# Kernel optimization log

Measured on AMD Instinct MI355X. Metric: run time of the kernel, lower is better.

The kernel has to match this reference:

```python
import jax, jax.numpy as jnp
import numpy as np

C = 1024      # channels
K = 7         # kernel_size
G = 1         # groups (G>1 crashes in the original torch code; see notes)
GC = C // G   # group_channels
OFFSET_SCALE = 2.0
LN_EPS = 1e-5


def setup_inputs() -> dict:
    key = jax.random.key(0)
    ks = jax.random.split(key, 8)
    N, L = 4, 2048
    s = 1.0 / np.sqrt(C)
    x = jax.random.normal(ks[0], (N, L, C), jnp.float32)
    Wi = jax.random.normal(ks[1], (C, C), jnp.float32) * s
    bi = jnp.zeros((C,), jnp.float32)
    dw_w = jax.random.normal(ks[2], (C, 1, 3), jnp.float32) * 0.5   # depthwise conv kernel (O, I/g=1, W)
    dw_b = jnp.zeros((C,), jnp.float32)
    ln_g = jnp.ones((C,), jnp.float32)
    ln_b = jnp.zeros((C,), jnp.float32)
    Wo = jax.random.normal(ks[3], (G * K, C), jnp.float32) * 0.02   # offset head (nonzero to exercise gather)
    bo = jnp.zeros((G * K,), jnp.float32)
    Wm = jax.random.normal(ks[4], (G * K, C), jnp.float32) * 0.02   # mask head
    bm = jnp.zeros((G * K,), jnp.float32)
    Wout = jax.random.normal(ks[5], (C, C), jnp.float32) * s
    bout = jnp.zeros((C,), jnp.float32)
    return {"x": x, "Wi": Wi, "bi": bi, "dw_w": dw_w, "dw_b": dw_b,
            "ln_g": ln_g, "ln_b": ln_b, "Wo": Wo, "bo": bo,
            "Wm": Wm, "bm": bm, "Wout": Wout, "bout": bout}


def _forward(x, Wi, bi, dw_w, dw_b, ln_g, ln_b, Wo, bo, Wm, bm, Wout, bout):
    N, L, Cc = x.shape
    dt = x.dtype
    # input projection
    x_proj = x @ Wi.T + bi                                  # [N,L,C]
    # depthwise conv (k=3, pad=1, groups=C) -> LayerNorm(C) -> GELU(exact)
    y = jax.lax.conv_general_dilated(
        x.transpose(0, 2, 1), dw_w, window_strides=(1,), padding=((1, 1),),
        dimension_numbers=("NCH", "OIH", "NCH"), feature_group_count=Cc)
    x_dw = y.transpose(0, 2, 1) + dw_b                       # [N,L,C]
    mu = x_dw.mean(-1, keepdims=True)
    var = ((x_dw - mu) ** 2).mean(-1, keepdims=True)
    x_dw = (x_dw - mu) * jax.lax.rsqrt(var + LN_EPS) * ln_g + ln_b
    x_dw = jax.nn.gelu(x_dw, approximate=False)
    # dynamic offsets and sampling mask
    offsets = (x_dw @ Wo.T + bo).reshape(N, L, G, K) * OFFSET_SCALE
    mask = jax.nn.softmax((x_dw @ Wm.T + bm).reshape(N, L, G, K), axis=-1)
    mask = jnp.nan_to_num(mask, nan=0.0)
    # absolute sampling positions
    ref_off = jnp.linspace(-(K // 2), K // 2, K).astype(dt)          # [K]
    pos = jnp.arange(L, dtype=dt)[None, :, None, None]               # [1,L,1,1]
    abs_pos = pos + ref_off[None, None, None, :] + offsets           # [N,L,G,K]
    apc = jnp.clip(abs_pos, 0.0, L - 1)
    p_floor = jnp.clip(apc.astype(jnp.int32), 0, L - 1)
    p_ceil = jnp.clip(p_floor + 1, 0, L - 1)
    w_ceil = apc - p_floor.astype(dt)
    w_floor = 1.0 - w_ceil
    valid = jnp.logical_not((abs_pos < 0) | (abs_pos > L - 1)).astype(dt)
    w_floor = w_floor * valid
    w_ceil = w_ceil * valid
    # gather + bilinear blend (G=1: each sample index grabs the full C channels)
    idx_f = p_floor.reshape(N, -1)[:, :, None]                       # [N, L*G*K, 1]
    idx_c = p_ceil.reshape(N, -1)[:, :, None]
    v_floor = jnp.take_along_axis(x_proj, idx_f, axis=1).reshape(N, L, G, K, GC)
    v_ceil = jnp.take_along_axis(x_proj, idx_c, axis=1).reshape(N, L, G, K, GC)
    sampled = v_floor * w_floor[..., None] + v_ceil * w_ceil[..., None]
    out = (sampled * mask[..., None]).sum(axis=3).reshape(N, L, Cc)  # sum over K
    return out @ Wout.T + bout


def reference(x, Wi, bi, dw_w, dw_b, ln_g, ln_b, Wo, bo, Wm, bm, Wout, bout):
    return _forward(x, Wi, bi, dw_w, dw_b, ln_g, ln_b, Wo, bo, Wm, bm, Wout, bout)
```

## Files before the change

### kernel.cpp

```cpp
#include <hip/hip_runtime.h>
#include <hip/hip_bf16.h>
#include <cstdint>

#define C_DIM 1024
#define L_DIM 2048
#define N_DIM 4
#define M_DIM (N_DIM * L_DIM)

typedef __attribute__((ext_vector_type(8))) short frag8;
typedef __attribute__((ext_vector_type(4)))  float f32x4;
typedef __attribute__((ext_vector_type(16))) float f32x16;

__device__ __forceinline__ void gl_lds16(const void* g, void* l) {
  __builtin_amdgcn_global_load_lds((const __attribute__((address_space(1))) void*)g,
                                   (__attribute__((address_space(3))) void*)l,
                                   16, 0, 0);
}
__device__ __forceinline__ void store_out(float* Y, size_t idx, float v) { Y[idx] = v; }
__device__ __forceinline__ void store_out(__hip_bfloat16* Y, size_t idx, float v) {
  Y[idx] = __float2bfloat16(v);
}
__device__ __forceinline__ float4 ldbf4(const __hip_bfloat16* p) {
  union { short4 s; __hip_bfloat16 h[4]; } u; u.s = *(const short4*)p;
  return make_float4((float)u.h[0], (float)u.h[1], (float)u.h[2], (float)u.h[3]);
}
__device__ __forceinline__ void stbf4(__hip_bfloat16* p, float4 v) {
  union { short4 s; __hip_bfloat16 h[4]; } u;
  u.h[0] = __float2bfloat16(v.x); u.h[1] = __float2bfloat16(v.y);
  u.h[2] = __float2bfloat16(v.z); u.h[3] = __float2bfloat16(v.w);
  *(short4*)p = u.s;
}
__device__ __forceinline__ float gelu_fast(float t) {
  const float t3 = t * t * t;
  const float ns = -1.5957691216f * t - 0.0713548163f * t3;
  return t / (1.f + __expf(ns));
}

__global__ __launch_bounds__(256)
void cvt_f32_bf16(const float* __restrict__ in, __hip_bfloat16* __restrict__ out, int n8) {
  const int i = blockIdx.x * 256 + threadIdx.x;
  if (i >= n8) return;
  const float4 a = *(const float4*)(in + (size_t)i * 8);
  const float4 b = *(const float4*)(in + (size_t)i * 8 + 4);
  union { __hip_bfloat16 h[8]; int4 q; } u;
  u.h[0] = __float2bfloat16(a.x); u.h[1] = __float2bfloat16(a.y);
  u.h[2] = __float2bfloat16(a.z); u.h[3] = __float2bfloat16(a.w);
  u.h[4] = __float2bfloat16(b.x); u.h[5] = __float2bfloat16(b.y);
  u.h[6] = __float2bfloat16(b.z); u.h[7] = __float2bfloat16(b.w);
  *(int4*)(out + (size_t)i * 8) = u.q;
}

__global__ __launch_bounds__(256)
void cvt_two_f32_bf16(const float* __restrict__ inA, __hip_bfloat16* __restrict__ outA,
                      const float* __restrict__ inB, __hip_bfloat16* __restrict__ outB,
                      int n8each) {
  int i = blockIdx.x * 256 + threadIdx.x;
  const float* in; __hip_bfloat16* out;
  if (i < n8each) { in = inA; out = outA; }
  else            { in = inB; out = outB; i -= n8each; }
  if (i >= n8each) return;
  const float4 a = *(const float4*)(in + (size_t)i * 8);
  const float4 b = *(const float4*)(in + (size_t)i * 8 + 4);
  union { __hip_bfloat16 h[8]; int4 q; } u;
  u.h[0] = __float2bfloat16(a.x); u.h[1] = __float2bfloat16(a.y);
  u.h[2] = __float2bfloat16(a.z); u.h[3] = __float2bfloat16(a.w);
  u.h[4] = __float2bfloat16(b.x); u.h[5] = __float2bfloat16(b.y);
  u.h[6] = __float2bfloat16(b.z); u.h[7] = __float2bfloat16(b.w);
  *(int4*)(out + (size_t)i * 8) = u.q;
}

template <typename TY>
__global__ __launch_bounds__(256, 2)
void gemm_db(const __hip_bfloat16* __restrict__ X,
             const __hip_bfloat16* __restrict__ W,
             const float* __restrict__ bias,
             TY* __restrict__ Y, int M, int N, int K)
{
  __shared__ __hip_bfloat16 As[2][2][128 * 32];
  __shared__ __hip_bfloat16 Bs[2][2][128 * 32];
  const int tid  = threadIdx.x;
  const int lane = tid & 63;
  const int wave = tid >> 6;
  const int bm = blockIdx.x * 128;
  const int bn = blockIdx.y * 128;
  const int wr = (wave >> 1) * 64;
  const int wc = (wave & 1) * 64;
  const int srow  = tid >> 2;
  const int skoff = (tid & 3) * 8;

  const __hip_bfloat16* gA0 = X + (size_t)(bm + srow) * K + skoff;
  const __hip_bfloat16* gA1 = X + (size_t)(bm + 64 + srow) * K + skoff;
  const __hip_bfloat16* gB0 = W + (size_t)(bn + srow) * K + skoff;
  const __hip_bfloat16* gB1 = W + (size_t)(bn + 64 + srow) * K + skoff;

  f32x16 acc[2][2] = {};
  const int arow  = lane & 31;
  const int akoff = (lane >> 5) * 8;

#define STAGE(k0, buf)                                        \
  do {                                                        \
    gl_lds16(gA0 + (k0),      &As[buf][0][tid * 8]);          \
    gl_lds16(gA1 + (k0),      &As[buf][0][2048 + tid * 8]);   \
    gl_lds16(gA0 + (k0) + 32, &As[buf][1][tid * 8]);          \
    gl_lds16(gA1 + (k0) + 32, &As[buf][1][2048 + tid * 8]);   \
    gl_lds16(gB0 + (k0),      &Bs[buf][0][tid * 8]);          \
    gl_lds16(gB1 + (k0),      &Bs[buf][0][2048 + tid * 8]);   \
    gl_lds16(gB0 + (k0) + 32, &Bs[buf][1][tid * 8]);          \
    gl_lds16(gB1 + (k0) + 32, &Bs[buf][1][2048 + tid * 8]);   \
  } while (0)

  STAGE(0, 0);
  __syncthreads();
  const int iters = K / 64;
  for (int it = 0; it < iters; ++it) {
    const int cur = it & 1;
    if (it + 1 < iters) STAGE((it + 1) * 64, cur ^ 1);

#pragma unroll
    for (int p = 0; p < 2; ++p)
#pragma unroll
      for (int h = 0; h < 2; ++h) {
        const frag8 a0 = *(const frag8*)&As[cur][p][(wr + arow) * 32 + h * 16 + akoff];
        const frag8 a1 = *(const frag8*)&As[cur][p][(wr + 32 + arow) * 32 + h * 16 + akoff];
        const frag8 b0 = *(const frag8*)&Bs[cur][p][(wc + arow) * 32 + h * 16 + akoff];
        const frag8 b1 = *(const frag8*)&Bs[cur][p][(wc + 32 + arow) * 32 + h * 16 + akoff];
        acc[0][0] = __builtin_amdgcn_mfma_f32_32x32x16_bf16(a0, b0, acc[0][0], 0, 0, 0);
        acc[0][1] = __builtin_amdgcn_mfma_f32_32x32x16_bf16(a0, b1, acc[0][1], 0, 0, 0);
        acc[1][0] = __builtin_amdgcn_mfma_f32_32x32x16_bf16(a1, b0, acc[1][0], 0, 0, 0);
        acc[1][1] = __builtin_amdgcn_mfma_f32_32x32x16_bf16(a1, b1, acc[1][1], 0, 0, 0);
      }
    __syncthreads();
  }
#undef STAGE

#pragma unroll
  for (int i = 0; i < 2; i++)
#pragma unroll
    for (int j = 0; j < 2; j++) {
      const int col = bn + wc + j * 32 + (lane & 31);
      const float bv = bias[col];
#pragma unroll
      for (int r = 0; r < 16; r++) {
        const int row = bm + wr + i * 32 + (r & 3) + 8 * (r >> 2) + 4 * (lane >> 5);
        store_out(Y, (size_t)row * N + col, acc[i][j][r] + bv);
      }
    }
}

struct Ld8f { float4 a, b; };
struct Ld8b { int4 a; };
__device__ __forceinline__ Ld8f ld8(const float* p) {
  return { *(const float4*)p, *(const float4*)(p + 4) };
}
__device__ __forceinline__ Ld8b ld8(const __hip_bfloat16* p) { return { *(const int4*)p }; }
__device__ __forceinline__ void st8(__hip_bfloat16* l, const Ld8f& v) {
  union { __hip_bfloat16 h[8]; int4 q; } u;
  u.h[0] = __float2bfloat16(v.a.x); u.h[1] = __float2bfloat16(v.a.y);
  u.h[2] = __float2bfloat16(v.a.z); u.h[3] = __float2bfloat16(v.a.w);
  u.h[4] = __float2bfloat16(v.b.x); u.h[5] = __float2bfloat16(v.b.y);
  u.h[6] = __float2bfloat16(v.b.z); u.h[7] = __float2bfloat16(v.b.w);
  *(int4*)l = u.q;
}
__device__ __forceinline__ void st8(__hip_bfloat16* l, const Ld8b& v) { *(int4*)l = v.a; }

template <typename TX, typename TY>
__global__ __launch_bounds__(256, 2)
void gemm_nt(const TX* __restrict__ X, const float* __restrict__ W,
             const float* __restrict__ bias, TY* __restrict__ Y, int M, int N, int K)
{
  __shared__ __hip_bfloat16 As[128 * 32];
  __shared__ __hip_bfloat16 Bs[128 * 32];
  const int tid  = threadIdx.x;
  const int lane = tid & 63;
  const int wave = tid >> 6;
  const int bm = blockIdx.x * 128;
  const int bn = blockIdx.y * 128;
  const int wr = (wave >> 1) * 64;
  const int wc = (wave & 1) * 64;
  const int srow  = tid >> 2;
  const int skoff = (tid & 3) * 8;

  f32x4 acc[4][4] = {};
  const TX*    gA0 = X + (size_t)(bm + srow) * K + skoff;
  const TX*    gA1 = X + (size_t)(bm + 64 + srow) * K + skoff;
  const float* gB0 = W + (size_t)(bn + srow) * K + skoff;
  const float* gB1 = W + (size_t)(bn + 64 + srow) * K + skoff;
  const int arow  = lane & 15;
  const int akoff = (lane >> 4) * 8;

  for (int k0 = 0; k0 < K; k0 += 32) {
    const auto va0 = ld8(gA0 + k0);
    const auto va1 = ld8(gA1 + k0);
    const auto vb0 = ld8(gB0 + k0);
    const auto vb1 = ld8(gB1 + k0);
    __syncthreads();
    st8(&As[srow * 32 + skoff],        va0);
    st8(&As[(64 + srow) * 32 + skoff], va1);
    st8(&Bs[srow * 32 + skoff],        vb0);
    st8(&Bs[(64 + srow) * 32 + skoff], vb1);
    __syncthreads();

    frag8 a[4], b[4];
#pragma unroll
    for (int i = 0; i < 4; i++)
      a[i] = *(const frag8*)&As[(wr + i * 16 + arow) * 32 + akoff];
#pragma unroll
    for (int j = 0; j < 4; j++)
      b[j] = *(const frag8*)&Bs[(wc + j * 16 + arow) * 32 + akoff];
#pragma unroll
    for (int i = 0; i < 4; i++)
#pragma unroll
      for (int j = 0; j < 4; j++)
        acc[i][j] = __builtin_amdgcn_mfma_f32_16x16x32_bf16(a[i], b[j], acc[i][j], 0, 0, 0);
  }
#pragma unroll
  for (int i = 0; i < 4; i++)
#pragma unroll
    for (int j = 0; j < 4; j++) {
      const int col = bn + wc + j * 16 + (lane & 15);
      const float bv = bias[col];
#pragma unroll
      for (int r = 0; r < 4; r++) {
        const int row = bm + wr + i * 16 + (lane >> 4) * 4 + r;
        store_out(Y, (size_t)row * N + col, acc[i][j][r] + bv);
      }
    }
}

__global__ __launch_bounds__(512, 2)
void pre_fused_v4(const float* __restrict__ x,
                  const float* __restrict__ dw_w, const float* __restrict__ dw_b,
                  const float* __restrict__ ln_g, const float* __restrict__ ln_b,
                  const float* __restrict__ Wo,   const float* __restrict__ bo,
                  const float* __restrict__ Wm,   const float* __restrict__ bmb,
                  __hip_bfloat16* __restrict__ xbb,
                  float* __restrict__ coef)
{
  __shared__ float sW[16384];
  float* sWo  = sW;
  float* sWm  = sW + 7168;
  float* slng = sW + 14336;
  float* slnb = sW + 15360;

  const int tid  = threadIdx.x;
  const int lane = tid & 63;
  const int wid  = tid >> 6;

#pragma unroll
  for (int i = 0; i < 3; i++) {
    gl_lds16(Wo + (size_t)(i * 512 + tid) * 4, &sWo[(i * 512 + tid) * 4]);
    gl_lds16(Wm + (size_t)(i * 512 + tid) * 4, &sWm[(i * 512 + tid) * 4]);
  }
  if (tid < 256) {
    gl_lds16(Wo + (size_t)(1536 + tid) * 4, &sWo[(1536 + tid) * 4]);
    gl_lds16(Wm + (size_t)(1536 + tid) * 4, &sWm[(1536 + tid) * 4]);
    gl_lds16(ln_g + (size_t)tid * 4, &slng[tid * 4]);
  } else {
    const int t = tid - 256;
    gl_lds16(ln_b + (size_t)t * 4, &slnb[t * 4]);
  }
  __syncthreads();

  const int b    = blockIdx.x;
  const int bs   = (b & 7) * 64 + (b >> 3);
  const int row0 = bs * 16 + wid * 2;
  const int l0   = row0 & (L_DIM - 1);

  const float* xr = x + (size_t)row0 * C_DIM;

  float4 v[2][4];
#pragma unroll
  for (int j = 0; j < 4; j++) {
    const int c4 = j * 256 + lane * 4;
    float4 xv[4];
#pragma unroll
    for (int m = 0; m < 4; m++) {
      const int lm = l0 + m - 1;
      if (lm >= 0 && lm < L_DIM)
        xv[m] = *(const float4*)(xr + ((long)m - 1) * C_DIM + c4);
      else
        xv[m] = make_float4(0.f, 0.f, 0.f, 0.f);
    }
#pragma unroll
    for (int r = 0; r < 2; r++)
      stbf4(xbb + (size_t)(row0 + r) * C_DIM + c4, xv[r + 1]);

    const float4 w0 = *(const float4*)(dw_w + (size_t)c4 * 3);
    const float4 w1 = *(const float4*)(dw_w + (size_t)c4 * 3 + 4);
    const float4 w2 = *(const float4*)(dw_w + (size_t)c4 * 3 + 8);
    const float4 bb = *(const float4*)(dw_b + c4);
#pragma unroll
    for (int r = 0; r < 2; r++) {
      const float4 xm = xv[r], x0 = xv[r + 1], xq = xv[r + 2];
      v[r][j].x = xm.x * w0.x + x0.x * w0.y + xq.x * w0.z + bb.x;
      v[r][j].y = xm.y * w0.w + x0.y * w1.x + xq.y * w1.y + bb.y;
      v[r][j].z = xm.z * w1.z + x0.z * w1.w + xq.z * w2.x + bb.z;
      v[r][j].w = xm.w * w2.y + x0.w * w2.z + xq.w * w2.w + bb.w;
    }
  }

  float mu[2], rstd[2];
#pragma unroll
  for (int r = 0; r < 2; r++) {
    float s1 = 0.f, s2 = 0.f;
#pragma unroll
    for (int j = 0; j < 4; j++) {
      s1 += v[r][j].x + v[r][j].y + v[r][j].z + v[r][j].w;
      s2 += v[r][j].x * v[r][j].x + v[r][j].y * v[r][j].y
          + v[r][j].z * v[r][j].z + v[r][j].w * v[r][j].w;
    }
    const float t1 = s1 + __shfl_xor(s1, 32);
    const float t2 = s2 + __shfl_xor(s2, 32);
    float cc = (lane < 32) ? t1 : t2;
#pragma unroll
    for (int m = 16; m >= 1; m >>= 1) cc += __shfl_xor(cc, m);
    const float dd = __shfl_xor(cc, 32);
    const float S1 = (lane < 32) ? cc : dd;
    const float S2 = (lane < 32) ? dd : cc;
    mu[r]   = S1 * (1.f / C_DIM);
    rstd[r] = rsqrtf(S2 * (1.f / C_DIM) - mu[r] * mu[r] + 1e-5f);
  }

  float po[2][7] = {}, pm[2][7] = {};
#pragma unroll
  for (int j = 0; j < 4; j++) {
    const int c4 = j * 256 + lane * 4;
    const float4 gg = *(const float4*)&slng[c4];
    const float4 bb = *(const float4*)&slnb[c4];
    float4 g[2];
#pragma unroll
    for (int r = 0; r < 2; r++) {
      g[r].x = gelu_fast((v[r][j].x - mu[r]) * rstd[r] * gg.x + bb.x);
      g[r].y = gelu_fast((v[r][j].y - mu[r]) * rstd[r] * gg.y + bb.y);
      g[r].z = gelu_fast((v[r][j].z - mu[r]) * rstd[r] * gg.z + bb.z);
      g[r].w = gelu_fast((v[r][j].w - mu[r]) * rstd[r] * gg.w + bb.w);
    }
#pragma unroll
    for (int k = 0; k < 7; k++) {
      const float4 wo = *(const float4*)&sWo[k * 1024 + c4];
      const float4 wm = *(const float4*)&sWm[k * 1024 + c4];
#pragma unroll
      for (int r = 0; r < 2; r++) {
        po[r][k] += g[r].x * wo.x + g[r].y * wo.y + g[r].z * wo.z + g[r].w * wo.w;
        pm[r][k] += g[r].x * wm.x + g[r].y * wm.y + g[r].z * wm.z + g[r].w * wm.w;
      }
    }
  }

  float poS[2][7], pmS[2][7];
#pragma unroll
  for (int r = 0; r < 2; r++)
#pragma unroll
    for (int k = 0; k < 7; k++) {
      const float tp = po[r][k] + __shfl_xor(po[r][k], 32);
      const float tm = pm[r][k] + __shfl_xor(pm[r][k], 32);
      float cc = (lane < 32) ? tp : tm;
#pragma unroll
      for (int m = 16; m >= 1; m >>= 1) cc += __shfl_xor(cc, m);
      const float dd = __shfl_xor(cc, 32);
      poS[r][k] = (lane < 32) ? cc : dd;
      pmS[r][k] = (lane < 32) ? dd : cc;
    }

#pragma unroll
  for (int r = 0; r < 2; r++) {
    float lg[7], mx = -1e30f;
#pragma unroll
    for (int k = 0; k < 7; k++) { lg[k] = pmS[r][k] + bmb[k]; mx = fmaxf(mx, lg[k]); }
    float se = 0.f, e[7];
#pragma unroll
    for (int k = 0; k < 7; k++) { e[k] = __expf(lg[k] - mx); se += e[k]; }
    const float inv = 1.f / se;
    const int l = l0 + r;

    if (lane == r) {
      float pk[32];
#pragma unroll
      for (int k = 0; k < 7; k++) {
        const float msk = e[k] * inv;
        const float off = (poS[r][k] + bo[k]) * 2.0f;
        const float ap  = (float)l + (float)(k - 3) + off;
        const float apc = fminf(fmaxf(ap, 0.f), (float)(L_DIM - 1));
        int f = (int)apc;
        int c = f + 1; if (c > L_DIM - 1) c = L_DIM - 1;
        const float w1  = apc - (float)f;
        const float val = (ap < 0.f || ap > (float)(L_DIM - 1)) ? 0.f : 1.f;
        pk[k]      = (1.f - w1) * val * msk;
        pk[8 + k]  = w1 * val * msk;
        pk[16 + k] = (float)f;
        pk[24 + k] = (float)c;
      }
      pk[7] = pk[15] = pk[23] = pk[31] = 0.f;
      float* cr = coef + (size_t)(row0 + r) * 32;
#pragma unroll
      for (int q = 0; q < 8; q++)
        *(float4*)(cr + q * 4) = make_float4(pk[q*4], pk[q*4+1], pk[q*4+2], pk[q*4+3]);
    }
  }
}

__global__ __launch_bounds__(256)
void gather_k(const float* __restrict__ coef,
              const __hip_bfloat16* __restrict__ xp,
              __hip_bfloat16* __restrict__ smp)
{
  const int b    = blockIdx.x;
  const int bs   = (b & 7) * 256 + (b >> 3);
  const int wid  = threadIdx.x >> 6;
  const int lane = threadIdx.x & 63;
  const int row  = bs * 4 + wid;
  const int n    = row >> 11;

  const float* cr = coef + (size_t)row * 32;
  const float4 q0 = *(const float4*)(cr);
  const float4 q1 = *(const float4*)(cr + 4);
  const float4 q2 = *(const float4*)(cr + 8);
  const float4 q3 = *(const float4*)(cr + 12);
  const float4 q4 = *(const float4*)(cr + 16);
  const float4 q5 = *(const float4*)(cr + 20);
  const float4 q6 = *(const float4*)(cr + 24);
  const float4 q7 = *(const float4*)(cr + 28);

  const float wf[7] = {q0.x, q0.y, q0.z, q0.w, q1.x, q1.y, q1.z};
  const float wc[7] = {q2.x, q2.y, q2.z, q2.w, q3.x, q3.y, q3.z};
  const int   pf[7] = {(int)q4.x, (int)q4.y, (int)q4.z, (int)q4.w, (int)q5.x, (int)q5.y, (int)q5.z};
  const int   pc[7] = {(int)q6.x, (int)q6.y, (int)q6.z, (int)q6.w, (int)q7.x, (int)q7.y, (int)q7.z};

  const __hip_bfloat16* xpn = xp + ((size_t)n * L_DIM) * C_DIM;
  __hip_bfloat16* so = smp + (size_t)row * C_DIM;

#pragma unroll
  for (int j = 0; j < 2; j++) {
    const int c8 = j * 512 + lane * 8;
    float a[8] = {0.f, 0.f, 0.f, 0.f, 0.f, 0.f, 0.f, 0.f};
#pragma unroll
    for (int k = 0; k < 7; k++) {
      union { int4 q; __hip_bfloat16 h[8]; } uf, uc;
      uf.q = *(const int4*)(xpn + (size_t)pf[k] * C_DIM + c8);
      uc.q = *(const int4*)(xpn + (size_t)pc[k] * C_DIM + c8);
#pragma unroll
      for (int t = 0; t < 8; t++)
        a[t] += wf[k] * (float)uf.h[t] + wc[k] * (float)uc.h[t];
    }
    union { int4 q; __hip_bfloat16 h[8]; } uo;
#pragma unroll
    for (int t = 0; t < 8; t++) uo.h[t] = __float2bfloat16(a[t]);
    *(int4*)(so + c8) = uo.q;
  }
}

__global__ __launch_bounds__(256)
void mid_fused_v4(const float* __restrict__ x,
                  const float* __restrict__ dw_w, const float* __restrict__ dw_b,
                  const float* __restrict__ ln_g, const float* __restrict__ ln_b,
                  const float* __restrict__ Wo,   const float* __restrict__ bo,
                  const float* __restrict__ Wm,   const float* __restrict__ bmb,
                  const __hip_bfloat16* __restrict__ xp,
                  __hip_bfloat16* __restrict__ smp)
{
  const int b    = blockIdx.x;
  const int bs   = (b & 7) * 256 + (b >> 3);
  const int wid  = threadIdx.x >> 6;
  const int lane = threadIdx.x & 63;
  const int row  = bs * 4 + wid;
  const int l    = row & (L_DIM - 1);
  const int n    = row >> 11;

  const float* xr = x + (size_t)row * C_DIM;

  float4 v[4];
#pragma unroll
  for (int j = 0; j < 4; j++) {
    const int c4 = j * 256 + lane * 4;
    const float4 x0 = *(const float4*)(xr + c4);
    float4 xm = make_float4(0.f, 0.f, 0.f, 0.f);
    float4 xq = make_float4(0.f, 0.f, 0.f, 0.f);
    if (l > 0)         xm = *(const float4*)(xr + c4 - C_DIM);
    if (l < L_DIM - 1) xq = *(const float4*)(xr + c4 + C_DIM);
    const float4 w0 = *(const float4*)(dw_w + (size_t)c4 * 3);
    const float4 w1 = *(const float4*)(dw_w + (size_t)c4 * 3 + 4);
    const float4 w2 = *(const float4*)(dw_w + (size_t)c4 * 3 + 8);
    const float4 bb = *(const float4*)(dw_b + c4);
    v[j].x = xm.x * w0.x + x0.x * w0.y + xq.x * w0.z + bb.x;
    v[j].y = xm.y * w0.w + x0.y * w1.x + xq.y * w1.y + bb.y;
    v[j].z = xm.z * w1.z + x0.z * w1.w + xq.z * w2.x + bb.z;
    v[j].w = xm.w * w2.y + x0.w * w2.z + xq.w * w2.w + bb.w;
  }

  float s1 = 0.f, s2 = 0.f;
#pragma unroll
  for (int j = 0; j < 4; j++) {
    s1 += v[j].x + v[j].y + v[j].z + v[j].w;
    s2 += v[j].x * v[j].x + v[j].y * v[j].y + v[j].z * v[j].z + v[j].w * v[j].w;
  }
#pragma unroll
  for (int m = 1; m < 64; m <<= 1) { s1 += __shfl_xor(s1, m); s2 += __shfl_xor(s2, m); }
  const float mu   = s1 * (1.f / C_DIM);
  const float rstd = rsqrtf(s2 * (1.f / C_DIM) - mu * mu + 1e-5f);

  float4 g[4];
#pragma unroll
  for (int j = 0; j < 4; j++) {
    const int c4 = j * 256 + lane * 4;
    const float4 gg = *(const float4*)(ln_g + c4);
    const float4 bb = *(const float4*)(ln_b + c4);
    g[j].x = gelu_fast((v[j].x - mu) * rstd * gg.x + bb.x);
    g[j].y = gelu_fast((v[j].y - mu) * rstd * gg.y + bb.y);
    g[j].z = gelu_fast((v[j].z - mu) * rstd * gg.z + bb.z);
    g[j].w = gelu_fast((v[j].w - mu) * rstd * gg.w + bb.w);
  }

  float po[7] = {0,0,0,0,0,0,0}, pm[7] = {0,0,0,0,0,0,0};
#pragma unroll
  for (int k = 0; k < 7; k++) {
#pragma unroll
    for (int j = 0; j < 4; j++) {
      const int c4 = j * 256 + lane * 4;
      const float4 wo = *(const float4*)(Wo + (size_t)k * C_DIM + c4);
      const float4 wm = *(const float4*)(Wm + (size_t)k * C_DIM + c4);
      po[k] += g[j].x * wo.x + g[j].y * wo.y + g[j].z * wo.z + g[j].w * wo.w;
      pm[k] += g[j].x * wm.x + g[j].y * wm.y + g[j].z * wm.z + g[j].w * wm.w;
    }
  }
#pragma unroll
  for (int k = 0; k < 7; k++)
#pragma unroll
    for (int m = 1; m < 64; m <<= 1) {
      po[k] += __shfl_xor(po[k], m);
      pm[k] += __shfl_xor(pm[k], m);
    }

  float lg[7], mx = -1e30f;
#pragma unroll
  for (int k = 0; k < 7; k++) { lg[k] = pm[k] + bmb[k]; mx = fmaxf(mx, lg[k]); }
  float se = 0.f, e[7];
#pragma unroll
  for (int k = 0; k < 7; k++) { e[k] = __expf(lg[k] - mx); se += e[k]; }
  const float inv = 1.f / se;

  float wf[7], wcl[7]; int pf[7], pc[7];
#pragma unroll
  for (int k = 0; k < 7; k++) {
    const float msk = e[k] * inv;
    const float off = (po[k] + bo[k]) * 2.0f;
    const float ap  = (float)l + (float)(k - 3) + off;
    const float apc = fminf(fmaxf(ap, 0.f), (float)(L_DIM - 1));
    int f = (int)apc;
    int c = f + 1; if (c > L_DIM - 1) c = L_DIM - 1;
    const float w1  = apc - (float)f;
    const float val = (ap < 0.f || ap > (float)(L_DIM - 1)) ? 0.f : 1.f;
    wf[k]  = (1.f - w1) * val * msk;
    wcl[k] = w1 * val * msk;
    pf[k] = f; pc[k] = c;
  }

  const __hip_bfloat16* xpn = xp + ((size_t)n * L_DIM) * C_DIM;
  __hip_bfloat16* so = smp + (size_t)row * C_DIM;
#pragma unroll
  for (int j = 0; j < 4; j++) {
    const int c4 = j * 256 + lane * 4;
    float4 a = make_float4(0.f, 0.f, 0.f, 0.f);
#pragma unroll
    for (int k = 0; k < 7; k++) {
      const float4 vf = ldbf4(xpn + (size_t)pf[k] * C_DIM + c4);
      const float4 vc = ldbf4(xpn + (size_t)pc[k] * C_DIM + c4);
      a.x += wf[k] * vf.x + wcl[k] * vc.x;
      a.y += wf[k] * vf.y + wcl[k] * vc.y;
      a.z += wf[k] * vf.z + wcl[k] * vc.z;
      a.w += wf[k] * vf.w + wcl[k] * vc.w;
    }
    stbf4(so + c4, a);
  }
}

extern "C" void kernel_launch(void* const* d_in, const int* in_sizes, int n_in,
                              void* d_out, int out_size, void* d_ws, size_t ws_size,
                              hipStream_t stream)
{
  const float* x    = (const float*)d_in[0];
  const float* Wi   = (const float*)d_in[1];
  const float* bi   = (const float*)d_in[2];
  const float* dw_w = (const float*)d_in[3];
  const float* dw_b = (const float*)d_in[4];
  const float* ln_g = (const float*)d_in[5];
  const float* ln_b = (const float*)d_in[6];
  const float* Wo   = (const float*)d_in[7];
  const float* bo   = (const float*)d_in[8];
  const float* Wm   = (const float*)d_in[9];
  const float* bm   = (const float*)d_in[10];
  const float* Wout = (const float*)d_in[11];
  const float* bout = (const float*)d_in[12];
  float* out = (float*)d_out;

  const size_t XE = (size_t)M_DIM * C_DIM;
  const size_t WE = (size_t)C_DIM * C_DIM;
  char* wsb = (char*)d_ws;
  __hip_bfloat16* xp    = (__hip_bfloat16*)wsb;
  __hip_bfloat16* smp   = (__hip_bfloat16*)(wsb + XE * 2);
  __hip_bfloat16* Wib   = (__hip_bfloat16*)(wsb + XE * 4);
  __hip_bfloat16* Woutb = (__hip_bfloat16*)(wsb + XE * 4 + WE * 2);
  __hip_bfloat16* xbb   = (__hip_bfloat16*)(wsb + XE * 4 + WE * 4);
  float*          coef  = (float*)(wsb + XE * 4 + WE * 4 + XE * 2);

  const size_t need_w2    = XE * 4 + WE * 4;
  const size_t need_full  = need_w2 + XE * 2;
  const size_t need_full2 = need_full + (size_t)M_DIM * 32 * 4;

  dim3 gg(M_DIM / 128, C_DIM / 128);

  if (ws_size >= need_full2) {
    cvt_two_f32_bf16<<<(int)(2 * (WE / 8) / 256), 256, 0, stream>>>(
        Wi, Wib, Wout, Woutb, (int)(WE / 8));
    pre_fused_v4<<<M_DIM / 16, 512, 0, stream>>>(x, dw_w, dw_b, ln_g, ln_b, Wo, bo, Wm, bm, xbb, coef);
    gemm_db<__hip_bfloat16><<<gg, 256, 0, stream>>>(xbb, Wib, bi, xp, M_DIM, C_DIM, C_DIM);
    gather_k<<<M_DIM / 4, 256, 0, stream>>>(coef, xp, smp);
    gemm_db<float><<<gg, 256, 0, stream>>>(smp, Woutb, bout, out, M_DIM, C_DIM, C_DIM);
  } else if (ws_size >= need_full) {
    cvt_f32_bf16<<<(int)(XE / 8 / 256), 256, 0, stream>>>(x, xbb, (int)(XE / 8));
    cvt_two_f32_bf16<<<(int)(2 * (WE / 8) / 256), 256, 0, stream>>>(
        Wi, Wib, Wout, Woutb, (int)(WE / 8));
    gemm_db<__hip_bfloat16><<<gg, 256, 0, stream>>>(xbb, Wib, bi, xp, M_DIM, C_DIM, C_DIM);
    mid_fused_v4<<<M_DIM / 4, 256, 0, stream>>>(x, dw_w, dw_b, ln_g, ln_b, Wo, bo, Wm, bm, xp, smp);
    gemm_db<float><<<gg, 256, 0, stream>>>(smp, Woutb, bout, out, M_DIM, C_DIM, C_DIM);
  } else if (ws_size >= need_w2) {
    cvt_f32_bf16<<<(int)(WE / 8 / 256), 256, 0, stream>>>(Wout, Woutb, (int)(WE / 8));
    gemm_nt<float, __hip_bfloat16><<<gg, 256, 0, stream>>>(x, Wi, bi, xp, M_DIM, C_DIM, C_DIM);
    mid_fused_v4<<<M_DIM / 4, 256, 0, stream>>>(x, dw_w, dw_b, ln_g, ln_b, Wo, bo, Wm, bm, xp, smp);
    gemm_db<float><<<gg, 256, 0, stream>>>(smp, Woutb, bout, out, M_DIM, C_DIM, C_DIM);
  } else {
    gemm_nt<float, __hip_bfloat16><<<gg, 256, 0, stream>>>(x, Wi, bi, xp, M_DIM, C_DIM, C_DIM);
    mid_fused_v4<<<M_DIM / 4, 256, 0, stream>>>(x, dw_w, dw_b, ln_g, ln_b, Wo, bo, Wm, bm, xp, smp);
    gemm_nt<__hip_bfloat16, float><<<gg, 256, 0, stream>>>(smp, Wout, bout, out, M_DIM, C_DIM, C_DIM);
  }
}
```

Baseline: 195.0 us.

## Fold input projection into output GEMM via precomputed Wout·Wi weight

Uses linearity of the gather-blend to apply it directly to bf16 x. The two large projections are replaced by a small 1024x1024 weight product Wout·Wi followed by a single large GEMM. The input bias is handled through per-row coefficient sums times Wout·bi, added in the GEMM epilogue. This removes one M×C×C GEMM and the x_proj intermediate, at the cost of extra bf16 rounding from the combined weight and a few small prep kernels.

```diff
diff --git a/kernel.cpp b/kernel.cpp
--- a/kernel.cpp
+++ b/kernel.cpp
@@ -69,12 +69,68 @@
   *(int4*)(out + (size_t)i * 8) = u.q;
 }
 
+__global__ __launch_bounds__(256)
+void cvt_trans_wi(const float* __restrict__ Wi, __hip_bfloat16* __restrict__ WiT) {
+  __shared__ float tile[64][65];
+  const int bi = blockIdx.x;
+  const int bj = blockIdx.y;
+  const int t  = threadIdx.x;
+  const int r  = t >> 2;
+  const int c0 = (t & 3) * 16;
+  const float* src = Wi + (size_t)(bi * 64 + r) * C_DIM + bj * 64 + c0;
+  *(float4*)&tile[r][c0]      = *(const float4*)(src);
+  *(float4*)&tile[r][c0 + 4]  = *(const float4*)(src + 4);
+  *(float4*)&tile[r][c0 + 8]  = *(const float4*)(src + 8);
+  *(float4*)&tile[r][c0 + 12] = *(const float4*)(src + 12);
+  __syncthreads();
+  const int kr = t >> 2, j0 = (t & 3) * 16;
+  __hip_bfloat16* dst = WiT + (size_t)(bj * 64 + kr) * C_DIM + bi * 64 + j0;
+  union { __hip_bfloat16 h[16]; int4 q[2]; } u;
+#pragma unroll
+  for (int i = 0; i < 16; i++) u.h[i] = __float2bfloat16(tile[j0 + i][kr]);
+  *(int4*)(dst)     = u.q[0];
+  *(int4*)(dst + 8) = u.q[1];
+}
+
+__global__ __launch_bounds__(256)
+void cvt_wout_bvec(const float* __restrict__ Wout, __hip_bfloat16* __restrict__ Woutb,
+                   const float* __restrict__ bi, float* __restrict__ bvec) {
+  const int b = blockIdx.x;
+  if (b < 512) {
+    const int i = b * 256 + threadIdx.x;
+    const float4 a = *(const float4*)(Wout + (size_t)i * 8);
+    const float4 c = *(const float4*)(Wout + (size_t)i * 8 + 4);
+    union { __hip_bfloat16 h[8]; int4 q; } u;
+    u.h[0] = __float2bfloat16(a.x); u.h[1] = __float2bfloat16(a.y);
+    u.h[2] = __float2bfloat16(a.z); u.h[3] = __float2bfloat16(a.w);
+    u.h[4] = __float2bfloat16(c.x); u.h[5] = __float2bfloat16(c.y);
+    u.h[6] = __float2bfloat16(c.z); u.h[7] = __float2bfloat16(c.w);
+    *(int4*)(Woutb + (size_t)i * 8) = u.q;
+  } else {
+    const int row  = (b - 512) * 4 + (threadIdx.x >> 6);
+    const int lane = threadIdx.x & 63;
+    const float* wr = Wout + (size_t)row * C_DIM;
+    float s = 0.f;
+#pragma unroll
+    for (int c = 0; c < 4; c++) {
+      const int j = c * 256 + lane * 4;
+      const float4 w  = *(const float4*)(wr + j);
+      const float4 bb = *(const float4*)(bi + j);
+      s += w.x * bb.x + w.y * bb.y + w.z * bb.z + w.w * bb.w;
+    }
+#pragma unroll
+    for (int m = 1; m < 64; m <<= 1) s += __shfl_xor(s, m);
+    if (lane == 0) bvec[row] = s;
+  }
+}
+
 template <typename TY>
 __global__ __launch_bounds__(256, 2)
 void gemm_db(const __hip_bfloat16* __restrict__ X,
              const __hip_bfloat16* __restrict__ W,
              const float* __restrict__ bias,
-             TY* __restrict__ Y, int M, int N, int K)
+             TY* __restrict__ Y, int M, int N, int K,
+             const float* __restrict__ sArr, const float* __restrict__ bvec)
 {
   __shared__ __hip_bfloat16 As[2][2][128 * 32];
   __shared__ __hip_bfloat16 Bs[2][2][128 * 32];
@@ -138,11 +194,14 @@
 #pragma unroll
     for (int j = 0; j < 2; j++) {
       const int col = bn + wc + j * 32 + (lane & 31);
-      const float bv = bias[col];
+      const float bv  = bias ? bias[col] : 0.f;
+      const float bvv = (sArr && bvec) ? bvec[col] : 0.f;
 #pragma unroll
       for (int r = 0; r < 16; r++) {
         const int row = bm + wr + i * 32 + (r & 3) + 8 * (r >> 2) + 4 * (lane >> 5);
-        store_out(Y, (size_t)row * N + col, acc[i][j][r] + bv);
+        float extra = bv;
+        if (sArr) extra += sArr[row] * bvv;
+        store_out(Y, (size_t)row * N + col, acc[i][j][r] + extra);
       }
     }
 }
@@ -400,9 +459,10 @@
 }
 
 __global__ __launch_bounds__(256)
-void gather_k(const float* __restrict__ coef,
-              const __hip_bfloat16* __restrict__ xp,
-              __hip_bfloat16* __restrict__ smp)
+void gather_g(const float* __restrict__ coef,
+              const __hip_bfloat16* __restrict__ xbb,
+              __hip_bfloat16* __restrict__ gb,
+              float* __restrict__ sArr)
 {
   const int b    = blockIdx.x;
   const int bs   = (b & 7) * 256 + (b >> 3);
@@ -426,8 +486,13 @@
   const int   pf[7] = {(int)q4.x, (int)q4.y, (int)q4.z, (int)q4.w, (int)q5.x, (int)q5.y, (int)q5.z};
   const int   pc[7] = {(int)q6.x, (int)q6.y, (int)q6.z, (int)q6.w, (int)q7.x, (int)q7.y, (int)q7.z};
 
-  const __hip_bfloat16* xpn = xp + ((size_t)n * L_DIM) * C_DIM;
-  __hip_bfloat16* so = smp + (size_t)row * C_DIM;
+  if (lane == 0) {
+    sArr[row] = q0.x + q0.y + q0.z + q0.w + q1.x + q1.y + q1.z
+              + q2.x + q2.y + q2.z + q2.w + q3.x + q3.y + q3.z;
+  }
+
+  const __hip_bfloat16* xpn = xbb + ((size_t)n * L_DIM) * C_DIM;
+  __hip_bfloat16* so = gb + (size_t)row * C_DIM;
 
 #pragma unroll
   for (int j = 0; j < 2; j++) {
@@ -595,38 +660,52 @@
   const size_t XE = (size_t)M_DIM * C_DIM;
   const size_t WE = (size_t)C_DIM * C_DIM;
   char* wsb = (char*)d_ws;
+
+  __hip_bfloat16* xbb2  = (__hip_bfloat16*)wsb;
+  __hip_bfloat16* gb    = (__hip_bfloat16*)(wsb + XE * 2);
+  __hip_bfloat16* Woutb2= (__hip_bfloat16*)(wsb + XE * 4);
+  __hip_bfloat16* WiT   = (__hip_bfloat16*)(wsb + XE * 4 + WE * 2);
+  __hip_bfloat16* Wcb   = (__hip_bfloat16*)(wsb + XE * 4 + WE * 4);
+  float* coef2 = (float*)(wsb + XE * 4 + WE * 6);
+  float* sArr  = (float*)(wsb + XE * 4 + WE * 6 + (size_t)M_DIM * 128);
+  float* bvec  = (float*)(wsb + XE * 4 + WE * 6 + (size_t)M_DIM * 128 + (size_t)M_DIM * 4);
+  const size_t need_v5 = XE * 4 + WE * 6 + (size_t)M_DIM * 132 + 4096;
+
   __hip_bfloat16* xp    = (__hip_bfloat16*)wsb;
   __hip_bfloat16* smp   = (__hip_bfloat16*)(wsb + XE * 2);
   __hip_bfloat16* Wib   = (__hip_bfloat16*)(wsb + XE * 4);
   __hip_bfloat16* Woutb = (__hip_bfloat16*)(wsb + XE * 4 + WE * 2);
   __hip_bfloat16* xbb   = (__hip_bfloat16*)(wsb + XE * 4 + WE * 4);
-  float*          coef  = (float*)(wsb + XE * 4 + WE * 4 + XE * 2);
-
-  const size_t need_w2    = XE * 4 + WE * 4;
-  const size_t need_full  = need_w2 + XE * 2;
-  const size_t need_full2 = need_full + (size_t)M_DIM * 32 * 4;
+  const size_t need_w2   = XE * 4 + WE * 4;
+  const size_t need_full = need_w2 + XE * 2;
 
   dim3 gg(M_DIM / 128, C_DIM / 128);
 
-  if (ws_size >= need_full2) {
-    cvt_two_f32_bf16<<<(int)(2 * (WE / 8) / 256), 256, 0, stream>>>(
-        Wi, Wib, Wout, Woutb, (int)(WE / 8));
-    pre_fused_v4<<<M_DIM / 16, 512, 0, stream>>>(x, dw_w, dw_b, ln_g, ln_b, Wo, bo, Wm, bm, xbb, coef);
-    gemm_db<__hip_bfloat16><<<gg, 256, 0, stream>>>(xbb, Wib, bi, xp, M_DIM, C_DIM, C_DIM);
-    gather_k<<<M_DIM / 4, 256, 0, stream>>>(coef, xp, smp);
-    gemm_db<float><<<gg, 256, 0, stream>>>(smp, Woutb, bout, out, M_DIM, C_DIM, C_DIM);
+  if (ws_size >= need_v5) {
+    cvt_trans_wi<<<dim3(16, 16), 256, 0, stream>>>(Wi, WiT);
+    cvt_wout_bvec<<<768, 256, 0, stream>>>(Wout, Woutb2, bi, bvec);
+    gemm_db<__hip_bfloat16><<<dim3(8, 8), 256, 0, stream>>>(
+        Woutb2, WiT, nullptr, Wcb, C_DIM, C_DIM, C_DIM, nullptr, nullptr);
+    pre_fused_v4<<<M_DIM / 16, 512, 0, stream>>>(
+        x, dw_w, dw_b, ln_g, ln_b, Wo, bo, Wm, bm, xbb2, coef2);
+    gather_g<<<M_DIM / 4, 256, 0, stream>>>(coef2, xbb2, gb, sArr);
+    gemm_db<float><<<gg, 256, 0, stream>>>(
+        gb, Wcb, bout, out, M_DIM, C_DIM, C_DIM, sArr, bvec);
   } else if (ws_size >= need_full) {
     cvt_f32_bf16<<<(int)(XE / 8 / 256), 256, 0, stream>>>(x, xbb, (int)(XE / 8));
     cvt_two_f32_bf16<<<(int)(2 * (WE / 8) / 256), 256, 0, stream>>>(
         Wi, Wib, Wout, Woutb, (int)(WE / 8));
-    gemm_db<__hip_bfloat16><<<gg, 256, 0, stream>>>(xbb, Wib, bi, xp, M_DIM, C_DIM, C_DIM);
+    gemm_db<__hip_bfloat16><<<gg, 256, 0, stream>>>(xbb, Wib, bi, xp, M_DIM, C_DIM, C_DIM,
+                                                    nullptr, nullptr);
     mid_fused_v4<<<M_DIM / 4, 256, 0, stream>>>(x, dw_w, dw_b, ln_g, ln_b, Wo, bo, Wm, bm, xp, smp);
-    gemm_db<float><<<gg, 256, 0, stream>>>(smp, Woutb, bout, out, M_DIM, C_DIM, C_DIM);
+    gemm_db<float><<<gg, 256, 0, stream>>>(smp, Woutb, bout, out, M_DIM, C_DIM, C_DIM,
+                                           nullptr, nullptr);
   } else if (ws_size >= need_w2) {
     cvt_f32_bf16<<<(int)(WE / 8 / 256), 256, 0, stream>>>(Wout, Woutb, (int)(WE / 8));
     gemm_nt<float, __hip_bfloat16><<<gg, 256, 0, stream>>>(x, Wi, bi, xp, M_DIM, C_DIM, C_DIM);
     mid_fused_v4<<<M_DIM / 4, 256, 0, stream>>>(x, dw_w, dw_b, ln_g, ln_b, Wo, bo, Wm, bm, xp, smp);
-    gemm_db<float><<<gg, 256, 0, stream>>>(smp, Woutb, bout, out, M_DIM, C_DIM, C_DIM);
+    gemm_db<float><<<gg, 256, 0, stream>>>(smp, Woutb, bout, out, M_DIM, C_DIM, C_DIM,
+                                           nullptr, nullptr);
   } else {
     gemm_nt<float, __hip_bfloat16><<<gg, 256, 0, stream>>>(x, Wi, bi, xp, M_DIM, C_DIM, C_DIM);
     mid_fused_v4<<<M_DIM / 4, 256, 0, stream>>>(x, dw_w, dw_b, ln_g, ln_b, Wo, bo, Wm, bm, xp, smp);
```

After: 201.9 us. 1.04x slower.
